# Optimization experiments

Measured on AMD Instinct MI355X. Metric: run time of the kernel, lower is better.

Reference implementation:

```python
import jax, jax.numpy as jnp
import numpy as np

N_NODES = 100000
N_EDGES = 1000000
IN_DIM = 128
HID = 128
OUT_DIM = 40


def setup_inputs() -> dict:
    key = jax.random.key(0)
    ks = jax.random.split(key, 16)
    x = jax.random.normal(ks[0], (N_NODES, IN_DIM), dtype=jnp.float32)
    edge_index = jax.random.randint(ks[1], (2, N_EDGES), 0, N_NODES, dtype=jnp.int64)
    s = 0.05
    # GAT layer 1 (in->hid, heads=1, concat=True)
    W1 = jax.random.normal(ks[2], (HID, IN_DIM), jnp.float32) * s
    b1 = jnp.zeros((HID,), jnp.float32)
    att1 = jax.random.normal(ks[3], (1, 2 * HID), jnp.float32) * s
    bias1 = jnp.zeros((HID,), jnp.float32)
    # GAT layer 2 (hid->hid)
    W2 = jax.random.normal(ks[4], (HID, HID), jnp.float32) * s
    b2 = jnp.zeros((HID,), jnp.float32)
    att2 = jax.random.normal(ks[5], (1, 2 * HID), jnp.float32) * s
    bias2 = jnp.zeros((HID,), jnp.float32)
    # post_mp: Linear(hid,hid) -> Dropout -> Linear(hid,out)
    Wp1 = jax.random.normal(ks[6], (HID, HID), jnp.float32) * s
    bp1 = jnp.zeros((HID,), jnp.float32)
    Wp2 = jax.random.normal(ks[7], (OUT_DIM, HID), jnp.float32) * s
    bp2 = jnp.zeros((OUT_DIM,), jnp.float32)
    return dict(x=x, edge_index=edge_index, W1=W1, b1=b1, att1=att1, bias1=bias1,
                W2=W2, b2=b2, att2=att2, bias2=bias2,
                Wp1=Wp1, bp1=bp1, Wp2=Wp2, bp2=bp2)


def gat_layer(x, src, dst, W, b, att, bias, n_nodes):
    # x: [N, Fin] -> h: [N, C] (heads=1, concat=True)
    h = x @ W.T + b
    C = h.shape[1]
    att_i, att_j = att[0, :C], att[0, C:]  # split: first half pairs with x_i (dst), second with x_j (src)
    # per-node scalar projections, then gather per edge (avoids [E,2C] concat)
    e = (h @ att_i)[dst] + (h @ att_j)[src]  # [E]
    e = jnp.where(e > 0, e, 0.2 * e)  # leaky_relu(0.2)
    # segment softmax over destination nodes
    m = jax.ops.segment_max(e, dst, num_segments=n_nodes)
    ex = jnp.exp(e - m[dst])
    denom = jax.ops.segment_sum(ex, dst, num_segments=n_nodes)
    alpha = ex / denom[dst]
    out = jax.ops.segment_sum(h[src] * alpha[:, None], dst, num_segments=n_nodes)
    return out + bias


def reference(x, edge_index, W1, b1, att1, bias1, W2, b2, att2, bias2, Wp1, bp1, Wp2, bp2):
    src, dst = edge_index[0], edge_index[1]
    n = x.shape[0]
    h = jax.nn.relu(gat_layer(x, src, dst, W1, b1, att1, bias1, n))  # dropout p=0 -> identity
    h = jax.nn.relu(gat_layer(h, src, dst, W2, b2, att2, bias2, n))
    y = (h @ Wp1.T + bp1) @ Wp2.T + bp2  # post_mp (eval: dropout identity)
    return jax.nn.log_softmax(y, axis=1)
```

## Files before the change

### kernel.cpp

```cpp
#include <hip/hip_runtime.h>

#define N_NODES 100000
#define N_EDGES 1000000
#define HID 128
#define OUT_DIM 40
#define CSR_W 64
#define CUR_STRIDE 16
#define GEMM_TILES 1563
#define G2_TILES 782
#define PROJ_TILES 1563
#define EDGE_BLK 977
#define WC_BLK 25

typedef __attribute__((ext_vector_type(8))) short bf16x8;
typedef __attribute__((ext_vector_type(8))) unsigned short u16x8;
typedef __attribute__((ext_vector_type(4))) float f32x4;

__device__ inline unsigned short f2bf(float f) {
    unsigned u = __float_as_uint(f);
    u += 0x7fffu + ((u >> 16) & 1u);
    return (unsigned short)(u >> 16);
}
__device__ inline float bf2f(unsigned short u) {
    return __uint_as_float(((unsigned)u) << 16);
}

__device__ inline float4 ld4(const float* p) { return *(const float4*)p; }

__global__ __launch_bounds__(256) void zero_conv_kernel(
    float4* __restrict__ p, int n4,
    const float* __restrict__ W1, const float* __restrict__ W2,
    unsigned short* __restrict__ W1b, unsigned short* __restrict__ W2b)
{
    if (blockIdx.x < 512) {
        int i = blockIdx.x * 256 + threadIdx.x;
        const int stride = 512 * 256;
        float4 z = make_float4(0.f, 0.f, 0.f, 0.f);
        for (; i < n4; i += stride) p[i] = z;
        return;
    }
    const int L = (blockIdx.x - 512) * 256 + threadIdx.x;
    const int e = L * 8;
    const float* s;
    unsigned short* d;
    if (e < HID * HID) { s = W1 + e; d = W1b + e; }
    else               { s = W2 + (e - HID * HID); d = W2b + (e - HID * HID); }
    float4 a = *(const float4*)s;
    float4 b = *(const float4*)(s + 4);
    ushort4 u0, u1;
    u0.x = f2bf(a.x); u0.y = f2bf(a.y); u0.z = f2bf(a.z); u0.w = f2bf(a.w);
    u1.x = f2bf(b.x); u1.y = f2bf(b.y); u1.z = f2bf(b.z); u1.w = f2bf(b.w);
    *(ushort4*)d = u0;
    *(ushort4*)(d + 4) = u1;
}

#define LDA 136
__device__ __forceinline__ void gemm_tile_body_f32(
    int tile, const float* __restrict__ A, const unsigned short* __restrict__ Wb,
    const float* __restrict__ out_bias, const float* __restrict__ att,
    unsigned short* __restrict__ Cb, float* __restrict__ hi, float* __restrict__ hj,
    int n_rows, unsigned short* As, unsigned short* Ws)
{
    const int t = threadIdx.x;
    const int row0 = tile * 64;

    for (int i = 0; i < 8; i++) {
        int lin = t + i * 256;
        int r = lin >> 5;
        int k = (lin & 31) * 4;
        int gr = row0 + r;
        float4 av = make_float4(0.f, 0.f, 0.f, 0.f);
        if (gr < n_rows) av = ld4(A + (size_t)gr * HID + k);
        ushort4 bv;
        bv.x = f2bf(av.x); bv.y = f2bf(av.y); bv.z = f2bf(av.z); bv.w = f2bf(av.w);
        *(ushort4*)(&As[r * LDA + k]) = bv;
    }
    for (int i = 0; i < 8; i++) {
        int lin = t + i * 256;
        int r = lin >> 4;
        int k = (lin & 15) * 8;
        *(bf16x8*)(&Ws[r * LDA + k]) = *(const bf16x8*)(Wb + (size_t)r * HID + k);
    }
    __syncthreads();

    const int wave = t >> 6, lane = t & 63;
    const int lrow = lane & 15, quad = lane >> 4;
    const int wrow = wave * 16;

    f32x4 acc[8];
    #pragma unroll
    for (int ni = 0; ni < 8; ni++) acc[ni] = (f32x4){0.f, 0.f, 0.f, 0.f};

    #pragma unroll
    for (int ks = 0; ks < 4; ks++) {
        const int kb = ks * 32 + quad * 8;
        bf16x8 af = *(bf16x8*)(&As[(wrow + lrow) * LDA + kb]);
        #pragma unroll
        for (int ni = 0; ni < 8; ni++) {
            bf16x8 bfr = *(bf16x8*)(&Ws[(ni * 16 + lrow) * LDA + kb]);
            acc[ni] = __builtin_amdgcn_mfma_f32_16x16x32_bf16(af, bfr, acc[ni], 0, 0, 0);
        }
    }

    float pi[4] = {0.f, 0.f, 0.f, 0.f}, pj[4] = {0.f, 0.f, 0.f, 0.f};
    const int rbase = row0 + wrow + quad * 4;
    #pragma unroll
    for (int ni = 0; ni < 8; ni++) {
        const int col = ni * 16 + lrow;
        const float bo = out_bias[col];
        const float ai = att[col], aj = att[HID + col];
        #pragma unroll
        for (int r = 0; r < 4; r++) {
            float v = acc[ni][r] + bo;
            int gr = rbase + r;
            if (gr < n_rows) Cb[(size_t)gr * HID + col] = f2bf(v);
            pi[r] = fmaf(v, ai, pi[r]);
            pj[r] = fmaf(v, aj, pj[r]);
        }
    }
    #pragma unroll
    for (int o = 1; o < 16; o <<= 1) {
        #pragma unroll
        for (int r = 0; r < 4; r++) {
            pi[r] += __shfl_xor(pi[r], o);
            pj[r] += __shfl_xor(pj[r], o);
        }
    }
    if (lrow == 0) {
        #pragma unroll
        for (int r = 0; r < 4; r++) {
            int gr = rbase + r;
            if (gr < n_rows) { hi[gr] = pi[r]; hj[gr] = pj[r]; }
        }
    }
}

__global__ __launch_bounds__(256) void combined_prep(
    const float* __restrict__ x, const unsigned short* __restrict__ W1b,
    const float* __restrict__ b1, const float* __restrict__ att1,
    const float* __restrict__ Wp1, const float* __restrict__ bp1,
    const float* __restrict__ Wp2, const float* __restrict__ bp2,
    const int* __restrict__ src, const int* __restrict__ dst,
    unsigned* __restrict__ cursor, int* __restrict__ csr,
    unsigned short* __restrict__ hbuf, float* __restrict__ hi, float* __restrict__ hj,
    unsigned short* __restrict__ Wcb, float* __restrict__ bc)
{
    __shared__ unsigned short As[64 * LDA];
    __shared__ unsigned short Ws[128 * LDA];
    const int b = blockIdx.x, g = b >> 3, r = b & 7;

    if (r < 3) {
        const int eid = g * 3 + r;
        if (eid >= EDGE_BLK) return;
        int e = eid * 1024 + threadIdx.x;
        #pragma unroll
        for (int j = 0; j < 4; j++, e += 256) {
            if (e < N_EDGES) {
                int d = dst[e], s = src[e];
                unsigned p = atomicAdd(&cursor[d << 4], 1u);
                if (p < CSR_W) __builtin_nontemporal_store(s, &csr[(d << 6) + p]);
            }
        }
        return;
    }
    const int oid = g * 5 + (r - 3);
    if (oid < WC_BLK) {
        int t = oid * 256 + threadIdx.x;
        if (t < OUT_DIM * HID) {
            int o = t >> 7, k = t & 127;
            float s = 0.f;
            for (int j = 0; j < HID; j++) s = fmaf(Wp2[o * HID + j], Wp1[j * HID + k], s);
            Wcb[t] = f2bf(s);
        } else if (t < 48 * HID) {
            Wcb[t] = 0;
        } else if (t < 48 * HID + OUT_DIM) {
            int o = t - 48 * HID;
            float s = bp2[o];
            for (int j = 0; j < HID; j++) s = fmaf(Wp2[o * HID + j], bp1[j], s);
            bc[o] = s;
        }
        return;
    }
    const int tile = oid - WC_BLK;
    if (tile >= GEMM_TILES) return;
    gemm_tile_body_f32(tile, x, W1b, b1, att1, hbuf, hi, hj, N_NODES, As, Ws);
}

__global__ __launch_bounds__(256) void gemm_mfma_b128(
    const unsigned short* __restrict__ A, const unsigned short* __restrict__ Wb,
    const float* __restrict__ out_bias, const float* __restrict__ att,
    unsigned short* __restrict__ Cb, float* __restrict__ hi, float* __restrict__ hj,
    int n_rows)
{
    __shared__ unsigned short As[128 * LDA];
    __shared__ unsigned short Ws[128 * LDA];
    const int t = threadIdx.x;
    const int row0 = blockIdx.x * 128;

    for (int i = 0; i < 8; i++) {
        int lin = t + i * 256;
        int r = lin >> 4;
        int k = (lin & 15) * 8;
        int gr = row0 + r;
        bf16x8 v = (bf16x8){0, 0, 0, 0, 0, 0, 0, 0};
        if (gr < n_rows) v = *(const bf16x8*)(A + (size_t)gr * HID + k);
        *(bf16x8*)(&As[r * LDA + k]) = v;
    }
    for (int i = 0; i < 8; i++) {
        int lin = t + i * 256;
        int r = lin >> 4;
        int k = (lin & 15) * 8;
        *(bf16x8*)(&Ws[r * LDA + k]) = *(const bf16x8*)(Wb + (size_t)r * HID + k);
    }
    __syncthreads();

    const int wave = t >> 6, lane = t & 63;
    const int lrow = lane & 15, quad = lane >> 4;

    f32x4 acc[2][8];
    #pragma unroll
    for (int mt = 0; mt < 2; mt++)
        #pragma unroll
        for (int ni = 0; ni < 8; ni++) acc[mt][ni] = (f32x4){0.f, 0.f, 0.f, 0.f};

    #pragma unroll
    for (int ks = 0; ks < 4; ks++) {
        const int kb = ks * 32 + quad * 8;
        bf16x8 af0 = *(bf16x8*)(&As[(wave * 32 + lrow) * LDA + kb]);
        bf16x8 af1 = *(bf16x8*)(&As[(wave * 32 + 16 + lrow) * LDA + kb]);
        #pragma unroll
        for (int ni = 0; ni < 8; ni++) {
            bf16x8 bfr = *(bf16x8*)(&Ws[(ni * 16 + lrow) * LDA + kb]);
            acc[0][ni] = __builtin_amdgcn_mfma_f32_16x16x32_bf16(af0, bfr, acc[0][ni], 0, 0, 0);
            acc[1][ni] = __builtin_amdgcn_mfma_f32_16x16x32_bf16(af1, bfr, acc[1][ni], 0, 0, 0);
        }
    }

    #pragma unroll
    for (int mt = 0; mt < 2; mt++) {
        float pi[4] = {0.f, 0.f, 0.f, 0.f}, pj[4] = {0.f, 0.f, 0.f, 0.f};
        const int rbase = row0 + wave * 32 + mt * 16 + quad * 4;
        #pragma unroll
        for (int ni = 0; ni < 8; ni++) {
            const int col = ni * 16 + lrow;
            const float bo = out_bias[col];
            const float ai = att[col], aj = att[HID + col];
            #pragma unroll
            for (int r = 0; r < 4; r++) {
                float v = acc[mt][ni][r] + bo;
                int gr = rbase + r;
                if (gr < n_rows) Cb[(size_t)gr * HID + col] = f2bf(v);
                pi[r] = fmaf(v, ai, pi[r]);
                pj[r] = fmaf(v, aj, pj[r]);
            }
        }
        #pragma unroll
        for (int o = 1; o < 16; o <<= 1) {
            #pragma unroll
            for (int r = 0; r < 4; r++) {
                pi[r] += __shfl_xor(pi[r], o);
                pj[r] += __shfl_xor(pj[r], o);
            }
        }
        if (lrow == 0) {
            #pragma unroll
            for (int r = 0; r < 4; r++) {
                int gr = rbase + r;
                if (gr < n_rows) { hi[gr] = pi[r]; hj[gr] = pj[r]; }
            }
        }
    }
}

__global__ __launch_bounds__(256) void fused_gat(
    const unsigned* __restrict__ cursor, const int* __restrict__ csr,
    const unsigned short* __restrict__ hb,
    const float* __restrict__ hi, const float* __restrict__ hj,
    const float* __restrict__ bias,
    unsigned short* __restrict__ out)
{
    const int wave = threadIdx.x >> 6;
    const int lane = threadIdx.x & 63;
    const int d = blockIdx.x * 4 + wave;
    if (d >= N_NODES) return;
    unsigned deg = cursor[d << 4];
    if (deg > CSR_W) deg = CSR_W;
    const int cnt = (int)deg;
    const float hid = hi[d];
    const int base = d << 6;

    int sv = 0;
    float ev = -INFINITY;
    if (lane < cnt) {
        sv = csr[base + lane];
        float e = hid + hj[sv];
        ev = e > 0.f ? e : 0.2f * e;
    }
    float m = ev;
    #pragma unroll
    for (int o = 32; o; o >>= 1) m = fmaxf(m, __shfl_xor(m, o));
    const float exv = (lane < cnt) ? __expf(ev - m) : 0.f;
    float denom = exv;
    #pragma unroll
    for (int o = 32; o; o >>= 1) denom += __shfl_xor(denom, o);

    const int g = lane >> 4;
    const int co = (lane & 15) * 8;
    float a[8];
    #pragma unroll
    for (int c = 0; c < 8; c++) a[c] = 0.f;

    if (cnt) {
        const int s0 = __shfl(sv, g);
        const int s1 = __shfl(sv, 4 + g);
        const int s2 = __shfl(sv, 8 + g);
        const int s3 = __shfl(sv, 12 + g);
        const u16x8 Q0 = *(const u16x8*)(hb + (size_t)s0 * HID + co);
        const u16x8 Q1 = *(const u16x8*)(hb + (size_t)s1 * HID + co);
        const u16x8 Q2 = *(const u16x8*)(hb + (size_t)s2 * HID + co);
        const u16x8 Q3 = *(const u16x8*)(hb + (size_t)s3 * HID + co);
        const float w0 = __shfl(exv, g);
        const float w1 = __shfl(exv, 4 + g);
        const float w2 = __shfl(exv, 8 + g);
        const float w3 = __shfl(exv, 12 + g);
        #pragma unroll
        for (int c = 0; c < 8; c++) {
            a[c] = fmaf(w0, bf2f(Q0[c]), a[c]);
            a[c] = fmaf(w1, bf2f(Q1[c]), a[c]);
            a[c] = fmaf(w2, bf2f(Q2[c]), a[c]);
            a[c] = fmaf(w3, bf2f(Q3[c]), a[c]);
        }
        for (int i = 16; i < cnt; i += 8) {
            const int e0 = i + g, e1 = i + 4 + g;
            const int t0 = __shfl(sv, e0);
            const int t1 = __shfl(sv, e1);
            const float v0 = __shfl(exv, e0);
            const float v1 = __shfl(exv, e1);
            const u16x8 p0 = *(const u16x8*)(hb + (size_t)t0 * HID + co);
            const u16x8 p1 = *(const u16x8*)(hb + (size_t)t1 * HID + co);
            #pragma unroll
            for (int c = 0; c < 8; c++) {
                a[c] = fmaf(v0, bf2f(p0[c]), a[c]);
                a[c] = fmaf(v1, bf2f(p1[c]), a[c]);
            }
        }
    }

    #pragma unroll
    for (int c = 0; c < 8; c++) {
        a[c] += __shfl_xor(a[c], 16);
        a[c] += __shfl_xor(a[c], 32);
    }

    const float inv = cnt ? 1.f / denom : 0.f;
    if (lane < 16) {
        const float4 bv0 = *(const float4*)(bias + co);
        const float4 bv1 = *(const float4*)(bias + co + 4);
        u16x8 o8;
        o8[0] = f2bf(fmaxf(fmaf(a[0], inv, bv0.x), 0.f));
        o8[1] = f2bf(fmaxf(fmaf(a[1], inv, bv0.y), 0.f));
        o8[2] = f2bf(fmaxf(fmaf(a[2], inv, bv0.z), 0.f));
        o8[3] = f2bf(fmaxf(fmaf(a[3], inv, bv0.w), 0.f));
        o8[4] = f2bf(fmaxf(fmaf(a[4], inv, bv1.x), 0.f));
        o8[5] = f2bf(fmaxf(fmaf(a[5], inv, bv1.y), 0.f));
        o8[6] = f2bf(fmaxf(fmaf(a[6], inv, bv1.z), 0.f));
        o8[7] = f2bf(fmaxf(fmaf(a[7], inv, bv1.w), 0.f));
        *(u16x8*)(out + (size_t)d * HID + co) = o8;
    }
}

__global__ __launch_bounds__(256) void final_proj_mfma(
    const unsigned short* __restrict__ agg,
    const unsigned short* __restrict__ Wcb, const float* __restrict__ bc,
    float* __restrict__ out)
{
    __shared__ unsigned short As[64 * LDA];
    __shared__ unsigned short Ws[48 * LDA];
    const int t = threadIdx.x;
    const int node0 = blockIdx.x * 64;

    for (int i = 0; i < 4; i++) {
        int lin = t + i * 256;
        int r = lin >> 4;
        int k = (lin & 15) * 8;
        int gr = node0 + r;
        bf16x8 v = (bf16x8){0, 0, 0, 0, 0, 0, 0, 0};
        if (gr < N_NODES) v = *(const bf16x8*)(agg + (size_t)gr * HID + k);
        *(bf16x8*)(&As[r * LDA + k]) = v;
    }
    for (int i = 0; i < 3; i++) {
        int lin = t + i * 256;
        int r = lin >> 4;
        int k = (lin & 15) * 8;
        *(bf16x8*)(&Ws[r * LDA + k]) = *(const bf16x8*)(Wcb + (size_t)r * HID + k);
    }
    __syncthreads();

    const int wave = t >> 6, lane = t & 63;
    const int lrow = lane & 15, quad = lane >> 4;
    const int wrow = wave * 16;

    f32x4 acc[3];
    #pragma unroll
    for (int nt = 0; nt < 3; nt++) acc[nt] = (f32x4){0.f, 0.f, 0.f, 0.f};

    #pragma unroll
    for (int ks = 0; ks < 4; ks++) {
        const int kb = ks * 32 + quad * 8;
        bf16x8 af = *(bf16x8*)(&As[(wrow + lrow) * LDA + kb]);
        #pragma unroll
        for (int nt = 0; nt < 3; nt++) {
            bf16x8 bfr = *(bf16x8*)(&Ws[(nt * 16 + lrow) * LDA + kb]);
            acc[nt] = __builtin_amdgcn_mfma_f32_16x16x32_bf16(af, bfr, acc[nt], 0, 0, 0);
        }
    }

    int cols[3]; float bcv[3]; bool valid[3];
    #pragma unroll
    for (int nt = 0; nt < 3; nt++) {
        cols[nt] = nt * 16 + lrow;
        valid[nt] = cols[nt] < OUT_DIM;
        bcv[nt] = valid[nt] ? bc[cols[nt]] : 0.f;
    }
    const int rbase = node0 + wrow + quad * 4;
    #pragma unroll
    for (int r = 0; r < 4; r++) {
        float v[3];
        float mx = -INFINITY;
        #pragma unroll
        for (int nt = 0; nt < 3; nt++) {
            v[nt] = acc[nt][r] + bcv[nt];
            if (valid[nt]) mx = fmaxf(mx, v[nt]);
        }
        #pragma unroll
        for (int o = 1; o < 16; o <<= 1) mx = fmaxf(mx, __shfl_xor(mx, o));
        float s = 0.f;
        #pragma unroll
        for (int nt = 0; nt < 3; nt++)
            if (valid[nt]) s += __expf(v[nt] - mx);
        #pragma unroll
        for (int o = 1; o < 16; o <<= 1) s += __shfl_xor(s, o);
        const float lse = mx + __logf(s);
        const int node = rbase + r;
        if (node < N_NODES) {
            #pragma unroll
            for (int nt = 0; nt < 3; nt++)
                if (valid[nt]) out[(size_t)node * OUT_DIM + cols[nt]] = v[nt] - lse;
        }
    }
}

extern "C" void kernel_launch(void* const* d_in, const int* in_sizes, int n_in,
                              void* d_out, int out_size, void* d_ws, size_t ws_size,
                              hipStream_t stream)
{
    const float* x     = (const float*)d_in[0];
    const int*   ei    = (const int*)d_in[1];
    const float* W1    = (const float*)d_in[2];
    const float* b1    = (const float*)d_in[3];
    const float* att1  = (const float*)d_in[4];
    const float* bias1 = (const float*)d_in[5];
    const float* W2    = (const float*)d_in[6];
    const float* b2    = (const float*)d_in[7];
    const float* att2  = (const float*)d_in[8];
    const float* bias2 = (const float*)d_in[9];
    const float* Wp1   = (const float*)d_in[10];
    const float* bp1   = (const float*)d_in[11];
    const float* Wp2   = (const float*)d_in[12];
    const float* bp2   = (const float*)d_in[13];
    float* out = (float*)d_out;

    const int* src = ei;
    const int* dst = ei + N_EDGES;

    char* ws = (char*)d_ws;
    unsigned short* hbuf = (unsigned short*)ws;
    unsigned short* aggb = hbuf + (size_t)N_NODES * HID;
    float* hi      = (float*)(aggb + (size_t)N_NODES * HID);
    float* hj      = hi + N_NODES;
    unsigned* cursor = (unsigned*)(hj + N_NODES);
    int* csr       = (int*)(cursor + (size_t)N_NODES * CUR_STRIDE);
    unsigned short* Wcb = (unsigned short*)(csr + (size_t)N_NODES * CSR_W);
    unsigned short* W1b = Wcb + 48 * HID;
    unsigned short* W2b = W1b + HID * HID;
    float* bc      = (float*)(W2b + HID * HID);

    const int prep_blocks = 326 * 8;

    zero_conv_kernel<<<528, 256, 0, stream>>>(
        (float4*)cursor, N_NODES * CUR_STRIDE / 4, W1, W2, W1b, W2b);

    combined_prep<<<prep_blocks, 256, 0, stream>>>(
        x, W1b, b1, att1, Wp1, bp1, Wp2, bp2, src, dst,
        cursor, csr, hbuf, hi, hj, Wcb, bc);

    fused_gat<<<N_NODES / 4, 256, 0, stream>>>(cursor, csr, hbuf, hi, hj, bias1, aggb);

    gemm_mfma_b128<<<G2_TILES, 256, 0, stream>>>(aggb, W2b, b2, att2, hbuf, hi, hj, N_NODES);
    fused_gat<<<N_NODES / 4, 256, 0, stream>>>(cursor, csr, hbuf, hi, hj, bias2, aggb);

    final_proj_mfma<<<PROJ_TILES, 256, 0, stream>>>(aggb, Wcb, bc, out);
}
```

Baseline: 296.6 us.

## Fuse second GAT aggregation into final projection kernel via LDS staging

The second-layer GAT aggregation is folded into the final projection kernel. Each wave aggregates 16 destination nodes one after another and writes the bf16 rows straight into shared memory as the MFMA A tile. This removes one kernel launch and the global write and re-read of the aggregated layer-2 features. In exchange, each block now handles only 64 nodes serially per wave (16 iterations), so gather latency is hidden by fewer independent blocks, and the larger kernel may reduce occupancy.

```diff
diff --git a/kernel.cpp b/kernel.cpp
--- a/kernel.cpp
+++ b/kernel.cpp
@@ -8,7 +8,7 @@
 #define CUR_STRIDE 16
 #define GEMM_TILES 1563
 #define G2_TILES 782
-#define PROJ_TILES 1563
+#define GP_TILES 1563
 #define EDGE_BLK 977
 #define WC_BLK 25
 
@@ -369,8 +369,11 @@
     }
 }
 
-__global__ __launch_bounds__(256) void final_proj_mfma(
-    const unsigned short* __restrict__ agg,
+__global__ __launch_bounds__(256) void gat_proj_mfma(
+    const unsigned* __restrict__ cursor, const int* __restrict__ csr,
+    const unsigned short* __restrict__ hb,
+    const float* __restrict__ hi, const float* __restrict__ hj,
+    const float* __restrict__ bias,
     const unsigned short* __restrict__ Wcb, const float* __restrict__ bc,
     float* __restrict__ out)
 {
@@ -379,24 +382,111 @@
     const int t = threadIdx.x;
     const int node0 = blockIdx.x * 64;
 
-    for (int i = 0; i < 4; i++) {
-        int lin = t + i * 256;
-        int r = lin >> 4;
-        int k = (lin & 15) * 8;
-        int gr = node0 + r;
-        bf16x8 v = (bf16x8){0, 0, 0, 0, 0, 0, 0, 0};
-        if (gr < N_NODES) v = *(const bf16x8*)(agg + (size_t)gr * HID + k);
-        *(bf16x8*)(&As[r * LDA + k]) = v;
-    }
     for (int i = 0; i < 3; i++) {
         int lin = t + i * 256;
         int r = lin >> 4;
         int k = (lin & 15) * 8;
         *(bf16x8*)(&Ws[r * LDA + k]) = *(const bf16x8*)(Wcb + (size_t)r * HID + k);
     }
+
+    const int wave = t >> 6;
+    const int lane = t & 63;
+    const int g = lane >> 4;
+    const int co = (lane & 15) * 8;
+    const float4 bv0 = *(const float4*)(bias + co);
+    const float4 bv1 = *(const float4*)(bias + co + 4);
+
+    for (int it = 0; it < 16; it++) {
+        const int rloc = (wave << 4) + it;
+        const int d = node0 + rloc;
+        if (d < N_NODES) {
+            unsigned deg = cursor[d << 4];
+            if (deg > CSR_W) deg = CSR_W;
+            const int cnt = (int)deg;
+            const float hid = hi[d];
+            const int base = d << 6;
+
+            int sv = 0;
+            float ev = -INFINITY;
+            if (lane < cnt) {
+                sv = csr[base + lane];
+                float e = hid + hj[sv];
+                ev = e > 0.f ? e : 0.2f * e;
+            }
+            float m = ev;
+            #pragma unroll
+            for (int o = 32; o; o >>= 1) m = fmaxf(m, __shfl_xor(m, o));
+            const float exv = (lane < cnt) ? __expf(ev - m) : 0.f;
+            float denom = exv;
+            #pragma unroll
+            for (int o = 32; o; o >>= 1) denom += __shfl_xor(denom, o);
+
+            float a[8];
+            #pragma unroll
+            for (int c = 0; c < 8; c++) a[c] = 0.f;
+
+            if (cnt) {
+                const int s0 = __shfl(sv, g);
+                const int s1 = __shfl(sv, 4 + g);
+                const int s2 = __shfl(sv, 8 + g);
+                const int s3 = __shfl(sv, 12 + g);
+                const u16x8 Q0 = *(const u16x8*)(hb + (size_t)s0 * HID + co);
+                const u16x8 Q1 = *(const u16x8*)(hb + (size_t)s1 * HID + co);
+                const u16x8 Q2 = *(const u16x8*)(hb + (size_t)s2 * HID + co);
+                const u16x8 Q3 = *(const u16x8*)(hb + (size_t)s3 * HID + co);
+                const float w0 = __shfl(exv, g);
+                const float w1 = __shfl(exv, 4 + g);
+                const float w2 = __shfl(exv, 8 + g);
+                const float w3 = __shfl(exv, 12 + g);
+                #pragma unroll
+                for (int c = 0; c < 8; c++) {
+                    a[c] = fmaf(w0, bf2f(Q0[c]), a[c]);
+                    a[c] = fmaf(w1, bf2f(Q1[c]), a[c]);
+                    a[c] = fmaf(w2, bf2f(Q2[c]), a[c]);
+                    a[c] = fmaf(w3, bf2f(Q3[c]), a[c]);
+                }
+                for (int i = 16; i < cnt; i += 8) {
+                    const int e0 = i + g, e1 = i + 4 + g;
+                    const int t0 = __shfl(sv, e0);
+                    const int t1 = __shfl(sv, e1);
+                    const float v0 = __shfl(exv, e0);
+                    const float v1 = __shfl(exv, e1);
+                    const u16x8 p0 = *(const u16x8*)(hb + (size_t)t0 * HID + co);
+                    const u16x8 p1 = *(const u16x8*)(hb + (size_t)t1 * HID + co);
+                    #pragma unroll
+                    for (int c = 0; c < 8; c++) {
+                        a[c] = fmaf(v0, bf2f(p0[c]), a[c]);
+                        a[c] = fmaf(v1, bf2f(p1[c]), a[c]);
+                    }
+                }
+            }
+
+            #pragma unroll
+            for (int c = 0; c < 8; c++) {
+                a[c] += __shfl_xor(a[c], 16);
+                a[c] += __shfl_xor(a[c], 32);
+            }
+
+            const float inv = cnt ? 1.f / denom : 0.f;
+            if (lane < 16) {
+                u16x8 o8;
+                o8[0] = f2bf(fmaxf(fmaf(a[0], inv, bv0.x), 0.f));
+                o8[1] = f2bf(fmaxf(fmaf(a[1], inv, bv0.y), 0.f));
+                o8[2] = f2bf(fmaxf(fmaf(a[2], inv, bv0.z), 0.f));
+                o8[3] = f2bf(fmaxf(fmaf(a[3], inv, bv0.w), 0.f));
+                o8[4] = f2bf(fmaxf(fmaf(a[4], inv, bv1.x), 0.f));
+                o8[5] = f2bf(fmaxf(fmaf(a[5], inv, bv1.y), 0.f));
+                o8[6] = f2bf(fmaxf(fmaf(a[6], inv, bv1.z), 0.f));
+                o8[7] = f2bf(fmaxf(fmaf(a[7], inv, bv1.w), 0.f));
+                *(u16x8*)(&As[rloc * LDA + co]) = o8;
+            }
+        } else if (lane < 16) {
+            u16x8 z = (u16x8){0, 0, 0, 0, 0, 0, 0, 0};
+            *(u16x8*)(&As[rloc * LDA + co]) = z;
+        }
+    }
     __syncthreads();
 
-    const int wave = t >> 6, lane = t & 63;
     const int lrow = lane & 15, quad = lane >> 4;
     const int wrow = wave * 16;
 
@@ -497,7 +587,7 @@
     fused_gat<<<N_NODES / 4, 256, 0, stream>>>(cursor, csr, hbuf, hi, hj, bias1, aggb);
 
     gemm_mfma_b128<<<G2_TILES, 256, 0, stream>>>(aggb, W2b, b2, att2, hbuf, hi, hj, N_NODES);
-    fused_gat<<<N_NODES / 4, 256, 0, stream>>>(cursor, csr, hbuf, hi, hj, bias2, aggb);
-
-    final_proj_mfma<<<PROJ_TILES, 256, 0, stream>>>(aggb, Wcb, bc, out);
-}
+
+    gat_proj_mfma<<<GP_TILES, 256, 0, stream>>>(
+        cursor, csr, hbuf, hi, hj, bias2, Wcb, bc, out);
+}
```

New measurement: 315.7 us. +6.4%, slower.
